# Performance work log

Hardware: AMD Instinct MI355X
Metric: run time of the kernel (lower is better)

Reference implementation:

```python
import jax, jax.numpy as jnp
import numpy as np

E, D_IN, D_OUT, T = 8, 2048, 8192, 16384


def setup_inputs() -> dict:
    key = jax.random.key(0)
    k1, k2 = jax.random.split(key, 2)
    inp = jax.random.normal(k1, (T, D_IN), dtype=jnp.float32)
    # kaiming-uniform-ish scale for weight [E, d_out, d_in]
    bound = float(1.0 / np.sqrt(D_IN))
    weight = jax.random.uniform(k2, (E, D_OUT, D_IN), dtype=jnp.float32,
                                minval=-bound, maxval=bound)
    bias = jnp.zeros((E, D_OUT), dtype=jnp.float32)
    # tokens are pre-sorted by expert; equal load here (2048 tokens/expert)
    fwd_expert_count = jnp.full((E,), T // E, dtype=jnp.int32)
    return {"inp": inp, "fwd_expert_count": fwd_expert_count,
            "weight": weight, "bias": bias}


def reference(inp, fwd_expert_count, weight, bias):
    # Grouped GEMM: expert e processes the contiguous slab of
    # fwd_expert_count[e] rows of inp; y = x_e @ W[e].T + b[e].
    counts = np.asarray(fwd_expert_count)          # concrete host ints
    offsets = np.concatenate([[0], np.cumsum(counts)])
    outs = []
    for e in range(counts.shape[0]):
        x_e = inp[offsets[e]:offsets[e + 1]]        # [c_e, d_in]
        outs.append(x_e @ weight[e].T + bias[e])    # [c_e, d_out]
    return jnp.concatenate(outs, axis=0)            # [T, d_out]
```

## Files before the change

kernel.cpp:

```cpp
#include <hip/hip_runtime.h>
#include <stdint.h>

typedef unsigned short u16;
typedef __attribute__((ext_vector_type(8))) short short8;
typedef __attribute__((ext_vector_type(4))) float f32x4;

#define NE   8
#define DIN  2048
#define DOUT 8192
#define NTOK 16384

__device__ __forceinline__ u16 f2bf(float f) {
  uint32_t u = __builtin_bit_cast(uint32_t, f);
  u += 0x7FFFu + ((u >> 16) & 1u);
  return (u16)(u >> 16);
}

__global__ __launch_bounds__(256) void cvt_f32_bf16(const float* __restrict__ src,
                                                    u16* __restrict__ dst, size_t n) {
  size_t i = ((size_t)blockIdx.x * 256 + threadIdx.x) * 8;
  const size_t stride = (size_t)gridDim.x * 256 * 8;
  for (; i < n; i += stride) {
    f32x4 a = *(const f32x4*)(src + i);
    f32x4 b = *(const f32x4*)(src + i + 4);
    short8 o;
    o[0] = (short)f2bf(a[0]); o[1] = (short)f2bf(a[1]);
    o[2] = (short)f2bf(a[2]); o[3] = (short)f2bf(a[3]);
    o[4] = (short)f2bf(b[0]); o[5] = (short)f2bf(b[1]);
    o[6] = (short)f2bf(b[2]); o[7] = (short)f2bf(b[3]);
    *(short8*)(dst + i) = o;
  }
}

#define GLOAD_LDS16(g, l) __builtin_amdgcn_global_load_lds( \
    (const __attribute__((address_space(1))) void*)(g),     \
    (__attribute__((address_space(3))) void*)(l), 16, 0, 0)

__global__ __launch_bounds__(512, 2) void moe_gemm8(
    const u16* __restrict__ Xb, const u16* __restrict__ Wb,
    const int* __restrict__ counts, const float* __restrict__ bias,
    float* __restrict__ C) {
  extern __shared__ u16 sm[];

  const int tid = threadIdx.x;
  const int l = tid & 63;
  const int wid = tid >> 6;
  const int wr = wid >> 2;
  const int wc = wid & 3;

  const int id = blockIdx.x;
  const int swz = (id & 7) * 256 + (id >> 3);
  const int e = swz >> 8;
  const int rem = swz & 255;
  const int tn = rem >> 3;
  const int tm = rem & 7;

  int off = 0;
  for (int i = 0; i < e; ++i) off += counts[i];
  const int row0 = off + tm * 256;
  const int col0 = tn * 256;
  const size_t wbase = (size_t)e * DOUT * DIN + (size_t)col0 * DIN;

  const int rl = l >> 2;
  const int q = (l & 3) ^ ((l >> 3) & 3);
  const int s0 = wid * 2, s1 = s0 + 1;
  const u16* pA0 = Xb + (size_t)(row0 + s0 * 16 + rl) * DIN + q * 8;
  const u16* pA1 = Xb + (size_t)(row0 + s1 * 16 + rl) * DIN + q * 8;
  const u16* pB0 = Wb + wbase + (size_t)(s0 * 16 + rl) * DIN + q * 8;
  const u16* pB1 = Wb + wbase + (size_t)(s1 * 16 + rl) * DIN + q * 8;

  const int f0 = ((l & 15) >> 1) & 3;
  const int gph = (l >> 4) ^ f0;
  const int aoff = (wr * 128 + (l & 15)) * 32 + gph * 8;
  const int boff = (wc * 64 + (l & 15)) * 32 + gph * 8;

  f32x4 acc[8][4] = {};
  short8 a[8], b0, b1;

#define SMA(buf, kh) (sm + (buf) * 32768 + (kh) * 8192)
#define SMB(buf, kh) (sm + (buf) * 32768 + 16384 + (kh) * 8192)
#define STAGE_A(buf, kt, kh) do { const int ko = (kt) * 64 + (kh) * 32; \
    GLOAD_LDS16(pA0 + ko, SMA(buf, kh) + s0 * 512);                     \
    GLOAD_LDS16(pA1 + ko, SMA(buf, kh) + s1 * 512); } while (0)
#define STAGE_B(buf, kt, kh) do { const int ko = (kt) * 64 + (kh) * 32; \
    GLOAD_LDS16(pB0 + ko, SMB(buf, kh) + s0 * 512);                     \
    GLOAD_LDS16(pB1 + ko, SMB(buf, kh) + s1 * 512); } while (0)
#define LDA(buf, kh) do { _Pragma("unroll") for (int m = 0; m < 8; ++m) \
    a[m] = *(const short8*)(SMA(buf, kh) + aoff + m * 512); } while (0)
#define LDB(buf, kh, n0) do {                                  \
    b0 = *(const short8*)(SMB(buf, kh) + boff + (n0) * 512);   \
    b1 = *(const short8*)(SMB(buf, kh) + boff + ((n0) + 1) * 512); } while (0)
#define FENCE() asm volatile("" ::: "memory")
#define BAR() do { FENCE(); __builtin_amdgcn_s_barrier(); FENCE(); } while (0)
#define VMW4() asm volatile("s_waitcnt vmcnt(4)" ::: "memory")
#define VMW0() asm volatile("s_waitcnt vmcnt(0)" ::: "memory")
#define MM(n0) do { __builtin_amdgcn_s_setprio(1); _Pragma("unroll")            \
    for (int m = 0; m < 8; ++m) {                                               \
      acc[m][n0] = __builtin_amdgcn_mfma_f32_16x16x32_bf16(a[m], b0, acc[m][n0], 0, 0, 0);             \
      acc[m][(n0) + 1] = __builtin_amdgcn_mfma_f32_16x16x32_bf16(a[m], b1, acc[m][(n0) + 1], 0, 0, 0); \
    }                                                                           \
    __builtin_amdgcn_s_setprio(0); } while (0)

  const int NKT = DIN / 64;

  STAGE_A(0, 0, 0); STAGE_B(0, 0, 0); STAGE_A(0, 0, 1); STAGE_B(0, 0, 1);
  VMW4();
  BAR();

  for (int kt = 0; kt < NKT; kt += 2) {
#define TILE(cur, nxt, t) do {                                  \
    const bool hn = (t) + 1 < NKT;                              \
                                         \
    LDA(cur, 0); LDB(cur, 0, 0);                                \
    if (hn) STAGE_A(nxt, (t) + 1, 0);                           \
    BAR(); MM(0); BAR();                                        \
                                         \
    LDB(cur, 0, 2);                                             \
    \
    if (hn) { STAGE_B(nxt, (t) + 1, 0); VMW4(); } else { VMW0(); } \
    BAR(); MM(2); BAR();                                        \
                                         \
    LDA(cur, 1); LDB(cur, 1, 0);                                \
    if (hn) STAGE_A(nxt, (t) + 1, 1);                           \
    BAR(); MM(0); BAR();                                        \
                                         \
    LDB(cur, 1, 2);                                             \
    if (hn) { STAGE_B(nxt, (t) + 1, 1); VMW4(); }               \
    BAR(); MM(2); BAR(); } while (0)
    TILE(0, 1, kt);
    TILE(1, 0, kt + 1);
#undef TILE
  }

  const int rb = row0 + wr * 128 + ((l >> 4) << 2);
  const int cb = col0 + wc * 64 + (l & 15);
#pragma unroll
  for (int n = 0; n < 4; ++n) {
    const int col = cb + n * 16;
    const float bv = bias[e * DOUT + col];
#pragma unroll
    for (int m = 0; m < 8; ++m) {
      const int r = rb + m * 16;
#pragma unroll
      for (int j = 0; j < 4; ++j)
        C[(size_t)(r + j) * DOUT + col] = acc[m][n][j] + bv;
    }
  }
}

__global__ __launch_bounds__(256) void moe_gemm_fused(
    const float* __restrict__ Xf, const float* __restrict__ Wf,
    const int* __restrict__ counts, const float* __restrict__ bias,
    float* __restrict__ C) {
  __shared__ __align__(16) u16 lds[2][2][128 * 32];

  const int tid = threadIdx.x;
  const int lane = tid & 63;
  const int wid = tid >> 6;
  const int wr = wid >> 1;
  const int wc = wid & 1;

  const int id = blockIdx.x;
  const int swz = (id & 7) * ((int)gridDim.x >> 3) + (id >> 3);
  const int e = swz >> 10;
  const int rem = swz & 1023;
  const int tn = rem >> 4;
  const int tml = rem & 15;

  int off = 0;
  for (int i = 0; i < e; ++i) off += counts[i];
  const int row0 = off + tml * 128;
  const int col0 = tn * 128;
  const size_t wbase = (size_t)e * DOUT * DIN + (size_t)col0 * DIN;

  f32x4 acc[4][4] = {};

  auto stage = [&](int buf, int kt) {
#pragma unroll
    for (int s = 0; s < 2; ++s) {
      int i = s * 256 + tid;
      int r = i >> 2, c = i & 3;
      const float* sa = Xf + (size_t)(row0 + r) * DIN + kt * 32 + c * 8;
      const float* sb = Wf + wbase + (size_t)r * DIN + kt * 32 + c * 8;
      f32x4 a0 = *(const f32x4*)sa;
      f32x4 a1 = *(const f32x4*)(sa + 4);
      f32x4 b0 = *(const f32x4*)sb;
      f32x4 b1 = *(const f32x4*)(sb + 4);
      short8 va, vb;
#pragma unroll
      for (int j = 0; j < 4; ++j) {
        va[j] = (short)f2bf(a0[j]); va[j + 4] = (short)f2bf(a1[j]);
        vb[j] = (short)f2bf(b0[j]); vb[j + 4] = (short)f2bf(b1[j]);
      }
      *(short8*)&lds[buf][0][i * 8] = va;
      *(short8*)&lds[buf][1][i * 8] = vb;
    }
  };

  auto compute = [&](int buf) {
    const int kc = lane >> 4;
    const int rr = lane & 15;
    short8 a[4], b[4];
    const u16* lA = lds[buf][0];
    const u16* lB = lds[buf][1];
#pragma unroll
    for (int m = 0; m < 4; ++m)
      a[m] = *(const short8*)(lA + (wr * 64 + m * 16 + rr) * 32 + kc * 8);
#pragma unroll
    for (int n = 0; n < 4; ++n)
      b[n] = *(const short8*)(lB + (wc * 64 + n * 16 + rr) * 32 + kc * 8);
#pragma unroll
    for (int m = 0; m < 4; ++m)
#pragma unroll
      for (int n = 0; n < 4; ++n)
        acc[m][n] = __builtin_amdgcn_mfma_f32_16x16x32_bf16(a[m], b[n], acc[m][n], 0, 0, 0);
  };

  stage(0, 0);
  for (int kt = 0; kt < DIN / 32; ++kt) {
    __syncthreads();
    if (kt + 1 < DIN / 32) stage((kt + 1) & 1, kt + 1);
    compute(kt & 1);
  }

  const int rbase = row0 + wr * 64;
  const int cbase = col0 + wc * 64;
#pragma unroll
  for (int n = 0; n < 4; ++n) {
    const int col = cbase + n * 16 + (lane & 15);
    const float bv = bias[e * DOUT + col];
#pragma unroll
    for (int m = 0; m < 4; ++m) {
      const int r0 = rbase + m * 16 + (lane >> 4) * 4;
#pragma unroll
      for (int j = 0; j < 4; ++j)
        C[(size_t)(r0 + j) * DOUT + col] = acc[m][n][j] + bv;
    }
  }
}

extern "C" void kernel_launch(void* const* d_in, const int* in_sizes, int n_in,
                              void* d_out, int out_size, void* d_ws, size_t ws_size,
                              hipStream_t stream) {
  const float* inp = (const float*)d_in[0];
  const int* counts = (const int*)d_in[1];
  const float* weight = (const float*)d_in[2];
  const float* bias = (const float*)d_in[3];
  float* out = (float*)d_out;

  const size_t nx = (size_t)NTOK * DIN;
  const size_t nw = (size_t)NE * DOUT * DIN;
  const size_t need = (nx + nw) * sizeof(u16);

  if (ws_size >= need) {
    u16* xb = (u16*)d_ws;
    u16* wb = xb + nx;
    cvt_f32_bf16<<<2048, 256, 0, stream>>>(inp, xb, nx);
    cvt_f32_bf16<<<2048, 256, 0, stream>>>(weight, wb, nw);
    const int grid = (NTOK / 256) * (DOUT / 256);
    moe_gemm8<<<grid, 512, 131072, stream>>>(xb, wb, counts, bias, out);
  } else {
    const int grid = (NTOK / 128) * (DOUT / 128);
    moe_gemm_fused<<<grid, 256, 0, stream>>>(inp, weight, counts, bias, out);
  }
}
```

Before: 802.7 us.

## Software-pipeline LDS fragment loads with MFMA and halve barriers per k-tile

Restructures the inner k-tile schedule to use separate register sets for A and B fragments. LDS reads for the next MFMA sub-block are issued before the current sub-block's MFMAs run. Barriers per tile drop from eight to four, and the global-to-LDS staging and vmcnt waits are re-placed. The goal is to hide LDS latency behind matrix instructions and cut barrier stalls. The cost is more fragment VGPRs and tighter ordering of async staging against LDS reuse.

```diff
diff --git a/kernel.cpp b/kernel.cpp
--- a/kernel.cpp
+++ b/kernel.cpp
@@ -75,7 +75,7 @@
   const int boff = (wc * 64 + (l & 15)) * 32 + gph * 8;
 
   f32x4 acc[8][4] = {};
-  short8 a[8], b0, b1;
+  short8 ax[8], ay[8], bp0, bp1, bq0, bq1, cp0, cp1, cq0, cq1;
 
 #define SMA(buf, kh) (sm + (buf) * 32768 + (kh) * 8192)
 #define SMB(buf, kh) (sm + (buf) * 32768 + 16384 + (kh) * 8192)
@@ -85,48 +85,53 @@
 #define STAGE_B(buf, kt, kh) do { const int ko = (kt) * 64 + (kh) * 32; \
     GLOAD_LDS16(pB0 + ko, SMB(buf, kh) + s0 * 512);                     \
     GLOAD_LDS16(pB1 + ko, SMB(buf, kh) + s1 * 512); } while (0)
-#define LDA(buf, kh) do { _Pragma("unroll") for (int m = 0; m < 8; ++m) \
-    a[m] = *(const short8*)(SMA(buf, kh) + aoff + m * 512); } while (0)
-#define LDB(buf, kh, n0) do {                                  \
-    b0 = *(const short8*)(SMB(buf, kh) + boff + (n0) * 512);   \
-    b1 = *(const short8*)(SMB(buf, kh) + boff + ((n0) + 1) * 512); } while (0)
+#define LDA8(arr, buf, kh) do { _Pragma("unroll") for (int m = 0; m < 8; ++m) \
+    arr[m] = *(const short8*)(SMA(buf, kh) + aoff + m * 512); } while (0)
+#define LDB2(v0, v1, buf, kh, n0) do {                          \
+    v0 = *(const short8*)(SMB(buf, kh) + boff + (n0) * 512);    \
+    v1 = *(const short8*)(SMB(buf, kh) + boff + ((n0) + 1) * 512); } while (0)
 #define FENCE() asm volatile("" ::: "memory")
 #define BAR() do { FENCE(); __builtin_amdgcn_s_barrier(); FENCE(); } while (0)
-#define VMW4() asm volatile("s_waitcnt vmcnt(4)" ::: "memory")
-#define VMW0() asm volatile("s_waitcnt vmcnt(0)" ::: "memory")
-#define MM(n0) do { __builtin_amdgcn_s_setprio(1); _Pragma("unroll")            \
-    for (int m = 0; m < 8; ++m) {                                               \
-      acc[m][n0] = __builtin_amdgcn_mfma_f32_16x16x32_bf16(a[m], b0, acc[m][n0], 0, 0, 0);             \
-      acc[m][(n0) + 1] = __builtin_amdgcn_mfma_f32_16x16x32_bf16(a[m], b1, acc[m][(n0) + 1], 0, 0, 0); \
-    }                                                                           \
+#define VMW(N) asm volatile("s_waitcnt vmcnt(" #N ")" ::: "memory")
+#define MM2(A, B0, B1, n0) do { __builtin_amdgcn_s_setprio(1); _Pragma("unroll")     \
+    for (int m = 0; m < 8; ++m) {                                                    \
+      acc[m][n0] = __builtin_amdgcn_mfma_f32_16x16x32_bf16(A[m], B0, acc[m][n0], 0, 0, 0);             \
+      acc[m][(n0) + 1] = __builtin_amdgcn_mfma_f32_16x16x32_bf16(A[m], B1, acc[m][(n0) + 1], 0, 0, 0); \
+    }                                                                                \
     __builtin_amdgcn_s_setprio(0); } while (0)
 
   const int NKT = DIN / 64;
 
   STAGE_A(0, 0, 0); STAGE_B(0, 0, 0); STAGE_A(0, 0, 1); STAGE_B(0, 0, 1);
-  VMW4();
+  VMW(4);
   BAR();
 
   for (int kt = 0; kt < NKT; kt += 2) {
-#define TILE(cur, nxt, t) do {                                  \
-    const bool hn = (t) + 1 < NKT;                              \
-                                         \
-    LDA(cur, 0); LDB(cur, 0, 0);                                \
-    if (hn) STAGE_A(nxt, (t) + 1, 0);                           \
-    BAR(); MM(0); BAR();                                        \
-                                         \
-    LDB(cur, 0, 2);                                             \
-    \
-    if (hn) { STAGE_B(nxt, (t) + 1, 0); VMW4(); } else { VMW0(); } \
-    BAR(); MM(2); BAR();                                        \
-                                         \
-    LDA(cur, 1); LDB(cur, 1, 0);                                \
-    if (hn) STAGE_A(nxt, (t) + 1, 1);                           \
-    BAR(); MM(0); BAR();                                        \
-                                         \
-    LDB(cur, 1, 2);                                             \
-    if (hn) { STAGE_B(nxt, (t) + 1, 1); VMW4(); }               \
-    BAR(); MM(2); BAR(); } while (0)
+#define TILE(cur, nxt, t) do {                                          \
+    const bool hn = (t) + 1 < NKT;                                      \
+             \
+    LDA8(ax, cur, 0);                                                   \
+    LDB2(bp0, bp1, cur, 0, 0);                                          \
+    if (hn) STAGE_A(nxt, (t) + 1, 0);                                   \
+    MM2(ax, bp0, bp1, 0);                                               \
+    LDB2(bq0, bq1, cur, 0, 2);                   \
+    if (hn) VMW(2); else VMW(0);     \
+    BAR();                                                              \
+               \
+    LDA8(ay, cur, 1);                  \
+    MM2(ax, bq0, bq1, 2);            \
+    LDB2(cp0, cp1, cur, 1, 0);                   \
+    if (hn) STAGE_B(nxt, (t) + 1, 0);                                   \
+    BAR();                                                              \
+                                                                \
+    MM2(ay, cp0, cp1, 0);                                               \
+    LDB2(cq0, cq1, cur, 1, 2);                   \
+    if (hn) STAGE_A(nxt, (t) + 1, 1);                                   \
+    BAR();                                                              \
+                                                                \
+    MM2(ay, cq0, cq1, 2);                                               \
+    if (hn) { STAGE_B(nxt, (t) + 1, 1); VMW(4); }                       \
+    BAR(); } while (0)
     TILE(0, 1, kt);
     TILE(1, 0, kt + 1);
 #undef TILE
```

After: 1.049 ms. 1.31x slower.
